# Optimization experiments

Hardware: AMD Instinct MI355X
Metric: run time of the kernel (lower is better)

The kernel has to match this reference:

```python
import jax, jax.numpy as jnp
import numpy as np

H, N, SEQ = 256, 64, 4096

def setup_inputs() -> dict:
    key = jax.random.key(0)
    kA, kB, kC, kdt = jax.random.split(key, 4)
    W = jax.random.normal(kA, (H, N, N), dtype=jnp.float32)
    # Hurwitz (stable) A: skew-symmetric part minus 0.5*I, like HiPPO-style stable transitions
    A = 0.5 * (W - jnp.swapaxes(W, -1, -2)) - 0.5 * jnp.eye(N, dtype=jnp.float32)
    B = jax.random.normal(kB, (H, N), dtype=jnp.float32)
    C = jax.random.normal(kC, (H, N), dtype=jnp.float32)
    # log_dt around log(0.01), matching typical S4 timescale init
    log_dt = jax.random.normal(kdt, (H,), dtype=jnp.float32) * 0.5 + jnp.log(0.01)
    return {"A": A, "B": B, "C": C, "log_dt": log_dt, "L": SEQ}

def _bilinear(dt, A, B):
    # dt: (H,), A: (H,N,N), B: (H,N)
    n = A.shape[-1]
    I = jnp.eye(n, dtype=A.dtype)
    A_back = I - (dt[:, None, None] / 2) * A   # (H,N,N)
    A_fwd = I + (dt[:, None, None] / 2) * A    # (H,N,N)
    dA = jnp.linalg.solve(A_back, A_fwd)                       # (H,N,N)
    dB = dt[:, None] * jnp.linalg.solve(A_back, B[..., None])[..., 0]  # (H,N)
    return dA, dB

def _krylov(L, dA, dB, C):
    # K[h, l] = C[h] @ dA[h]^l @ dB[h], computed by squaring/doubling
    x = dB[..., None]  # (H, N, 1)
    A_ = dA
    while x.shape[-1] < L:
        x2 = jnp.einsum('hmn,hnl->hml', A_, x)  # apply current power
        x = jnp.concatenate([x, x2], axis=-1)
        if x.shape[-1] < L:
            A_ = jnp.einsum('hmn,hnk->hmk', A_, A_)  # square the power
    x = x[..., :L]  # (H, N, L)
    return jnp.einsum('hn,hnl->hl', C, x)  # (H, L)

def reference(A, B, C, log_dt, L):
    dt = jnp.exp(log_dt)
    dA, dB = _bilinear(dt, A, B)
    return _krylov(L, dA, dB, C)
```

## Files before the change

### kernel.cpp

```cpp
#include <hip/hip_runtime.h>

constexpr int STRU = 68;

typedef short v8s __attribute__((ext_vector_type(8)));
typedef float v4f __attribute__((ext_vector_type(4)));

__device__ __forceinline__ unsigned packhl(float x) {
    unsigned xb = __builtin_bit_cast(unsigned, x);
    unsigned hb = xb & 0xffff0000u;
    float lof = x - __builtin_bit_cast(float, hb);
    unsigned lb = __builtin_bit_cast(unsigned, lof) + 0x8000u;
    return __builtin_amdgcn_perm(xb, lb, 0x07060302u);
}

__device__ __forceinline__ float unpackf(unsigned v) {
    float h = __builtin_bit_cast(float, v & 0xffff0000u);
    float l = __builtin_bit_cast(float, v << 16);
    return h + l;
}

__device__ __forceinline__ void load_frag(const unsigned* p, v8s& hi, v8s& lo) {
    uint4 a = *(const uint4*)p;
    uint4 b = *(const uint4*)(p + 4);
    uint4 hw, lw;
    hw.x = __builtin_amdgcn_perm(a.y, a.x, 0x07060302u);
    hw.y = __builtin_amdgcn_perm(a.w, a.z, 0x07060302u);
    hw.z = __builtin_amdgcn_perm(b.y, b.x, 0x07060302u);
    hw.w = __builtin_amdgcn_perm(b.w, b.z, 0x07060302u);
    lw.x = __builtin_amdgcn_perm(a.y, a.x, 0x05040100u);
    lw.y = __builtin_amdgcn_perm(a.w, a.z, 0x05040100u);
    lw.z = __builtin_amdgcn_perm(b.y, b.x, 0x05040100u);
    lw.w = __builtin_amdgcn_perm(b.w, b.z, 0x05040100u);
    hi = __builtin_bit_cast(v8s, hw);
    lo = __builtin_bit_cast(v8s, lw);
}

#define MFMA __builtin_amdgcn_mfma_f32_16x16x32_bf16

template<int MODE>
__device__ __forceinline__ void mm64(const unsigned* __restrict__ P,
                                     const unsigned* __restrict__ Q,
                                     unsigned* D, unsigned* DT, float* G,
                                     const unsigned* R, float ca, float cb,
                                     int tid) {
    const int lane = tid & 63, w = tid >> 6;
    const int nh = lane & 15, qh = lane >> 4;
    const int tr = w >> 1, tc0 = (w & 1) << 1;
    v4f acc[2] = {v4f{0,0,0,0}, v4f{0,0,0,0}};
    #pragma unroll
    for (int kk = 0; kk < 2; ++kk) {
        const int kc = kk * 32 + qh * 8;
        v8s ph, pl, q0h, q0l, q1h, q1l;
        load_frag(P + (tr * 16 + nh) * STRU + kc, ph, pl);
        load_frag(Q + (tc0 * 16 + nh) * STRU + kc, q0h, q0l);
        load_frag(Q + ((tc0 + 1) * 16 + nh) * STRU + kc, q1h, q1l);
        acc[0] = MFMA(ph, q0h, acc[0], 0, 0, 0);
        acc[0] = MFMA(ph, q0l, acc[0], 0, 0, 0);
        acc[0] = MFMA(pl, q0h, acc[0], 0, 0, 0);
        acc[1] = MFMA(ph, q1h, acc[1], 0, 0, 0);
        acc[1] = MFMA(ph, q1l, acc[1], 0, 0, 0);
        acc[1] = MFMA(pl, q1h, acc[1], 0, 0, 0);
    }
    const int row0 = tr * 16 + qh * 4;
    #pragma unroll
    for (int c = 0; c < 2; ++c) {
        const int col = (tc0 + c) * 16 + nh;
        if constexpr (MODE == 2) {
            #pragma unroll
            for (int e = 0; e < 4; ++e) G[(row0 + e) * 64 + col] = acc[c][e];
        } else if constexpr (MODE == 0) {
            #pragma unroll
            for (int e = 0; e < 4; ++e)
                D[(row0 + e) * STRU + col] = packhl(acc[c][e]);
        } else if constexpr (MODE == 1) {
            #pragma unroll
            for (int e = 0; e < 4; ++e) {
                float v = acc[c][e] + ((row0 + e) == col ? 1.0f : 0.0f);
                D[(row0 + e) * STRU + col] = packhl(v);
            }
        } else if constexpr (MODE == 3) {
            uint4 tp;
            #pragma unroll
            for (int e = 0; e < 4; ++e) {
                unsigned pk = packhl(acc[c][e]);
                D[(row0 + e) * STRU + col] = pk;
                ((unsigned*)&tp)[e] = pk;
            }
            *(uint4*)&DT[col * STRU + row0] = tp;
        } else if constexpr (MODE == 4) {
            #pragma unroll
            for (int e = 0; e < 4; ++e) {
                float dv = ca * acc[c][e];
                float dg = ((row0 + e) == col) ? 1.0f : 0.0f;
                D[(row0 + e) * STRU + col]  = packhl(dv);
                DT[(row0 + e) * STRU + col] = packhl(dv + dg);
            }
        } else if constexpr (MODE == 5) {
            #pragma unroll
            for (int e = 0; e < 4; ++e) {
                float t  = unpackf(R[(row0 + e) * STRU + col]);
                float dg = ((row0 + e) == col) ? 1.0f : 0.0f;
                float base = ca * t - dg;
                float sv   = cb * acc[c][e];
                D[(row0 + e) * STRU + col]  = packhl(base + sv);
                DT[(row0 + e) * STRU + col] = packhl(base - sv);
            }
        }
    }
}

__device__ __forceinline__ void dbl64(unsigned* Xt, const unsigned* M, int k, int tid) {
    const int lane = tid & 63, w = tid >> 6;
    const int nh = lane & 15, qh = lane >> 4;
    const int nt = (k + 15) >> 4;
    if (w < 4 * nt) {
        const int t = w >> 2, cb = w & 3;
        v4f acc = {0, 0, 0, 0};
        #pragma unroll
        for (int kk = 0; kk < 2; ++kk) {
            const int kc = kk * 32 + qh * 8;
            v8s ph, pl, mh, ml;
            load_frag(Xt + (t * 16 + nh) * STRU + kc, ph, pl);
            load_frag(M + (cb * 16 + nh) * STRU + kc, mh, ml);
            acc = MFMA(ph, mh, acc, 0, 0, 0);
            acc = MFMA(ph, ml, acc, 0, 0, 0);
            acc = MFMA(pl, mh, acc, 0, 0, 0);
        }
        #pragma unroll
        for (int e = 0; e < 4; ++e) {
            const int j = t * 16 + qh * 4 + e;
            if (j < k) Xt[(k + j) * STRU + cb * 16 + nh] = packhl(acc[e]);
        }
    }
}

__launch_bounds__(512)
__global__ void krylov_kernel(const float* __restrict__ A,
                              const float* __restrict__ Bv,
                              const float* __restrict__ Cv,
                              const float* __restrict__ logdt,
                              float* __restrict__ out)
{
    const int h    = blockIdx.x;
    const int tid  = threadIdx.x;
    const int lane = tid & 63;
    const int w    = tid >> 6;

    __shared__ __align__(16) unsigned SM[6][64 * STRU];
    __shared__ float Bl[64];

    const float dt = expf(logdt[h]);
    const float c  = 0.5f * dt;
    const float al = 1.0f + 0.5f * c;
    const float sd = -(c * c) / (al * al);
    const float c1 = 2.0f / al;
    const float c2 = 2.0f * c / (al * al);

    const float* Ah = A + (size_t)h * 4096;

    for (int idx = tid; idx < 1024; idx += 512) {
        const int r = idx >> 4, c0 = (idx & 15) * 4;
        float4 v = *(const float4*)(Ah + idx * 4);
        if (r == c0 + 0) v.x += 0.5f;
        if (r == c0 + 1) v.y += 0.5f;
        if (r == c0 + 2) v.z += 0.5f;
        if (r == c0 + 3) v.w += 0.5f;
        uint4 pk = make_uint4(packhl(v.x), packhl(v.y), packhl(v.z), packhl(v.w));
        *(uint4*)&SM[0][r * STRU + c0] = pk;
    }
    if (tid < 64) Bl[tid] = Bv[h * 64 + tid];
    else if (tid < 128) SM[5][tid - 64] = packhl(Cv[h * 64 + (tid - 64)]);
    __syncthreads();

    mm64<4>(SM[0], SM[0], SM[1], SM[2], nullptr, nullptr, sd, 0.f, tid);
    __syncthreads();
    mm64<1>(SM[1], SM[2], SM[3], nullptr, nullptr, nullptr, 0.f, 0.f, tid);
    __syncthreads();
    mm64<1>(SM[1], SM[3], SM[2], nullptr, nullptr, nullptr, 0.f, 0.f, tid);
    __syncthreads();
    mm64<1>(SM[1], SM[2], SM[3], nullptr, nullptr, nullptr, 0.f, 0.f, tid);
    __syncthreads();
    mm64<5>(SM[0], SM[3], SM[2], SM[1], nullptr, SM[3], c1, c2, tid);
    __syncthreads();

    if (w == 0) {
        const unsigned* Xr = SM[2] + lane * STRU;
        float acc = 0.0f;
        #pragma unroll
        for (int m4 = 0; m4 < 16; ++m4) {
            uint4 xv = *(const uint4*)(Xr + 4 * m4);
            float4 b4 = *(const float4*)&Bl[4 * m4];
            acc += unpackf(xv.x) * b4.x + unpackf(xv.y) * b4.y
                 + unpackf(xv.z) * b4.z + unpackf(xv.w) * b4.w;
        }
        SM[4][lane] = packhl(c * (acc + Bl[lane]));
    }
    __syncthreads();

    unsigned *bX = SM[2], *bXT = SM[1], *bN = SM[0], *bNT = SM[3];
    #pragma unroll 1
    for (int s = 0; s < 6; ++s) {
        mm64<3>(bX, bXT, bN, bNT, nullptr, nullptr, 0.f, 0.f, tid);
        dbl64(SM[4], bX, 1 << s, tid);
        __syncthreads();
        unsigned* t0 = bX;  bX  = bN;  bN  = t0;
        t0 = bXT; bXT = bNT; bNT = t0;
    }

    #pragma unroll 1
    for (int s = 0; s < 6; ++s) {
        if (s < 5) mm64<3>(bX, bXT, bN, bNT, nullptr, nullptr, 0.f, 0.f, tid);
        dbl64(SM[5], bXT, 1 << s, tid);
        __syncthreads();
        if (s < 5) {
            unsigned* t0 = bX;  bX  = bN;  bN  = t0;
            t0 = bXT; bXT = bNT; bNT = t0;
        }
    }

    mm64<2>(SM[5], SM[4], nullptr, nullptr, out + (size_t)h * 4096, nullptr,
            0.f, 0.f, tid);
}

extern "C" void kernel_launch(void* const* d_in, const int* in_sizes, int n_in,
                              void* d_out, int out_size, void* d_ws, size_t ws_size,
                              hipStream_t stream) {
    const float* A  = (const float*)d_in[0];
    const float* B  = (const float*)d_in[1];
    const float* C  = (const float*)d_in[2];
    const float* ld = (const float*)d_in[3];
    float* out = (float*)d_out;
    const int H = in_sizes[3];
    krylov_kernel<<<H, 512, 0, stream>>>(A, B, C, ld, out);
}
```

Before: 79.63 us.

## Restructure Krylov kernel with 1024 threads, swizzled LDS, column-fragment loads and fewer buffers

Rewrites the per-head kernel to launch 1024 threads so each wave computes one 16x16 tile, and replaces the padded LDS layout with an XOR-swizzled one. Transposed copies of matrices are dropped in favour of column-strided fragment loads. The LDS footprint shrinks from six to four matrix buffers. The dB solve is restructured into two matrix-vector products, and the two doubling loops are merged into one 12-step loop. MFMA accumulation is split across two accumulators. The aim is to cut LDS bank conflicts, transpose writes and LDS usage, and to raise parallelism per block, at the cost of strided scalar LDS reads for the column fragments and more threads contending at each barrier.

```diff
diff --git a/kernel.cpp b/kernel.cpp
--- a/kernel.cpp
+++ b/kernel.cpp
@@ -4,6 +4,10 @@
 
 typedef short v8s __attribute__((ext_vector_type(8)));
 typedef float v4f __attribute__((ext_vector_type(4)));
+
+__device__ __forceinline__ int swz(int i, int j) {
+    return i * STRU + (j ^ ((i & 8) << 1));
+}
 
 __device__ __forceinline__ unsigned packhl(float x) {
     unsigned xb = __builtin_bit_cast(unsigned, x);
@@ -35,106 +39,47 @@
     lo = __builtin_bit_cast(v8s, lw);
 }
 
-#define MFMA __builtin_amdgcn_mfma_f32_16x16x32_bf16
-
-template<int MODE>
-__device__ __forceinline__ void mm64(const unsigned* __restrict__ P,
-                                     const unsigned* __restrict__ Q,
-                                     unsigned* D, unsigned* DT, float* G,
-                                     const unsigned* R, float ca, float cb,
-                                     int tid) {
-    const int lane = tid & 63, w = tid >> 6;
-    const int nh = lane & 15, qh = lane >> 4;
-    const int tr = w >> 1, tc0 = (w & 1) << 1;
-    v4f acc[2] = {v4f{0,0,0,0}, v4f{0,0,0,0}};
+__device__ __forceinline__ void load_col_frag(const unsigned* Q, int col, int kbase,
+                                              v8s& hi, v8s& lo) {
+    unsigned x[8];
+    #pragma unroll
+    for (int j = 0; j < 8; ++j) x[j] = Q[swz(kbase + j, col)];
+    uint4 hw, lw;
+    hw.x = __builtin_amdgcn_perm(x[1], x[0], 0x07060302u);
+    hw.y = __builtin_amdgcn_perm(x[3], x[2], 0x07060302u);
+    hw.z = __builtin_amdgcn_perm(x[5], x[4], 0x07060302u);
+    hw.w = __builtin_amdgcn_perm(x[7], x[6], 0x07060302u);
+    lw.x = __builtin_amdgcn_perm(x[1], x[0], 0x05040100u);
+    lw.y = __builtin_amdgcn_perm(x[3], x[2], 0x05040100u);
+    lw.z = __builtin_amdgcn_perm(x[5], x[4], 0x05040100u);
+    lw.w = __builtin_amdgcn_perm(x[7], x[6], 0x05040100u);
+    hi = __builtin_bit_cast(v8s, hw);
+    lo = __builtin_bit_cast(v8s, lw);
+}
+
+#define MFMA16 __builtin_amdgcn_mfma_f32_16x16x32_bf16
+
+template<bool BCOL>
+__device__ __forceinline__ v4f tile16(const unsigned* __restrict__ P,
+                                      const unsigned* __restrict__ Q,
+                                      int rb, int cb, int lane) {
+    const int nh = lane & 15, qd = lane >> 4;
+    v4f a0 = {0, 0, 0, 0}, a1 = {0, 0, 0, 0};
     #pragma unroll
     for (int kk = 0; kk < 2; ++kk) {
-        const int kc = kk * 32 + qh * 8;
-        v8s ph, pl, q0h, q0l, q1h, q1l;
-        load_frag(P + (tr * 16 + nh) * STRU + kc, ph, pl);
-        load_frag(Q + (tc0 * 16 + nh) * STRU + kc, q0h, q0l);
-        load_frag(Q + ((tc0 + 1) * 16 + nh) * STRU + kc, q1h, q1l);
-        acc[0] = MFMA(ph, q0h, acc[0], 0, 0, 0);
-        acc[0] = MFMA(ph, q0l, acc[0], 0, 0, 0);
-        acc[0] = MFMA(pl, q0h, acc[0], 0, 0, 0);
-        acc[1] = MFMA(ph, q1h, acc[1], 0, 0, 0);
-        acc[1] = MFMA(ph, q1l, acc[1], 0, 0, 0);
-        acc[1] = MFMA(pl, q1h, acc[1], 0, 0, 0);
-    }
-    const int row0 = tr * 16 + qh * 4;
-    #pragma unroll
-    for (int c = 0; c < 2; ++c) {
-        const int col = (tc0 + c) * 16 + nh;
-        if constexpr (MODE == 2) {
-            #pragma unroll
-            for (int e = 0; e < 4; ++e) G[(row0 + e) * 64 + col] = acc[c][e];
-        } else if constexpr (MODE == 0) {
-            #pragma unroll
-            for (int e = 0; e < 4; ++e)
-                D[(row0 + e) * STRU + col] = packhl(acc[c][e]);
-        } else if constexpr (MODE == 1) {
-            #pragma unroll
-            for (int e = 0; e < 4; ++e) {
-                float v = acc[c][e] + ((row0 + e) == col ? 1.0f : 0.0f);
-                D[(row0 + e) * STRU + col] = packhl(v);
-            }
-        } else if constexpr (MODE == 3) {
-            uint4 tp;
-            #pragma unroll
-            for (int e = 0; e < 4; ++e) {
-                unsigned pk = packhl(acc[c][e]);
-                D[(row0 + e) * STRU + col] = pk;
-                ((unsigned*)&tp)[e] = pk;
-            }
-            *(uint4*)&DT[col * STRU + row0] = tp;
-        } else if constexpr (MODE == 4) {
-            #pragma unroll
-            for (int e = 0; e < 4; ++e) {
-                float dv = ca * acc[c][e];
-                float dg = ((row0 + e) == col) ? 1.0f : 0.0f;
-                D[(row0 + e) * STRU + col]  = packhl(dv);
-                DT[(row0 + e) * STRU + col] = packhl(dv + dg);
-            }
-        } else if constexpr (MODE == 5) {
-            #pragma unroll
-            for (int e = 0; e < 4; ++e) {
-                float t  = unpackf(R[(row0 + e) * STRU + col]);
-                float dg = ((row0 + e) == col) ? 1.0f : 0.0f;
-                float base = ca * t - dg;
-                float sv   = cb * acc[c][e];
-                D[(row0 + e) * STRU + col]  = packhl(base + sv);
-                DT[(row0 + e) * STRU + col] = packhl(base - sv);
-            }
-        }
-    }
-}
-
-__device__ __forceinline__ void dbl64(unsigned* Xt, const unsigned* M, int k, int tid) {
-    const int lane = tid & 63, w = tid >> 6;
-    const int nh = lane & 15, qh = lane >> 4;
-    const int nt = (k + 15) >> 4;
-    if (w < 4 * nt) {
-        const int t = w >> 2, cb = w & 3;
-        v4f acc = {0, 0, 0, 0};
-        #pragma unroll
-        for (int kk = 0; kk < 2; ++kk) {
-            const int kc = kk * 32 + qh * 8;
-            v8s ph, pl, mh, ml;
-            load_frag(Xt + (t * 16 + nh) * STRU + kc, ph, pl);
-            load_frag(M + (cb * 16 + nh) * STRU + kc, mh, ml);
-            acc = MFMA(ph, mh, acc, 0, 0, 0);
-            acc = MFMA(ph, ml, acc, 0, 0, 0);
-            acc = MFMA(pl, mh, acc, 0, 0, 0);
-        }
-        #pragma unroll
-        for (int e = 0; e < 4; ++e) {
-            const int j = t * 16 + qh * 4 + e;
-            if (j < k) Xt[(k + j) * STRU + cb * 16 + nh] = packhl(acc[e]);
-        }
-    }
-}
-
-__launch_bounds__(512)
+        const int kc = kk * 32 + qd * 8;
+        v8s ph, pl, qh, ql;
+        load_frag(P + swz(rb + nh, kc), ph, pl);
+        if constexpr (BCOL) load_col_frag(Q, cb + nh, kc, qh, ql);
+        else                load_frag(Q + swz(cb + nh, kc), qh, ql);
+        a0 = MFMA16(ph, qh, a0, 0, 0, 0);
+        a1 = MFMA16(ph, ql, a1, 0, 0, 0);
+        a1 = MFMA16(pl, qh, a1, 0, 0, 0);
+    }
+    return a0 + a1;
+}
+
+__launch_bounds__(1024)
 __global__ void krylov_kernel(const float* __restrict__ A,
                               const float* __restrict__ Bv,
                               const float* __restrict__ Cv,
@@ -145,81 +90,145 @@
     const int tid  = threadIdx.x;
     const int lane = tid & 63;
     const int w    = tid >> 6;
-
-    __shared__ __align__(16) unsigned SM[6][64 * STRU];
-    __shared__ float Bl[64];
-
-    const float dt = expf(logdt[h]);
-    const float c  = 0.5f * dt;
-    const float al = 1.0f + 0.5f * c;
-    const float sd = -(c * c) / (al * al);
-    const float c1 = 2.0f / al;
-    const float c2 = 2.0f * c / (al * al);
+    const int nh   = lane & 15, qd = lane >> 4;
+    const int rb   = (w >> 2) * 16, cb = (w & 3) * 16;
+
+    __shared__ __align__(16) unsigned W0[64 * STRU], W1[64 * STRU],
+                                      W2[64 * STRU], W3[64 * STRU];
+    __shared__ float Bl[64], Cl[64], tmv[64];
+
+    const float dt  = expf(logdt[h]);
+    const float c   = 0.5f * dt;
+    const float al  = 1.0f + 0.5f * c;
+    const float sd2 = (c * c) / (al * al);
+    const float c1  = 2.0f / al;
+    const float c2  = 2.0f * c / (al * al);
+    const float k1  = dt / al;
+    const float k2  = dt * c / (al * al);
 
     const float* Ah = A + (size_t)h * 4096;
 
-    for (int idx = tid; idx < 1024; idx += 512) {
-        const int r = idx >> 4, c0 = (idx & 15) * 4;
-        float4 v = *(const float4*)(Ah + idx * 4);
-        if (r == c0 + 0) v.x += 0.5f;
-        if (r == c0 + 1) v.y += 0.5f;
-        if (r == c0 + 2) v.z += 0.5f;
-        if (r == c0 + 3) v.w += 0.5f;
+    {
+        const int rr = tid >> 4, c0 = (tid & 15) * 4;
+        float4 v = *(const float4*)(Ah + rr * 64 + c0);
+        if (rr == c0 + 0) v.x += 0.5f;
+        if (rr == c0 + 1) v.y += 0.5f;
+        if (rr == c0 + 2) v.z += 0.5f;
+        if (rr == c0 + 3) v.w += 0.5f;
         uint4 pk = make_uint4(packhl(v.x), packhl(v.y), packhl(v.z), packhl(v.w));
-        *(uint4*)&SM[0][r * STRU + c0] = pk;
-    }
-    if (tid < 64) Bl[tid] = Bv[h * 64 + tid];
-    else if (tid < 128) SM[5][tid - 64] = packhl(Cv[h * 64 + (tid - 64)]);
-    __syncthreads();
-
-    mm64<4>(SM[0], SM[0], SM[1], SM[2], nullptr, nullptr, sd, 0.f, tid);
-    __syncthreads();
-    mm64<1>(SM[1], SM[2], SM[3], nullptr, nullptr, nullptr, 0.f, 0.f, tid);
-    __syncthreads();
-    mm64<1>(SM[1], SM[3], SM[2], nullptr, nullptr, nullptr, 0.f, 0.f, tid);
-    __syncthreads();
-    mm64<1>(SM[1], SM[2], SM[3], nullptr, nullptr, nullptr, 0.f, 0.f, tid);
-    __syncthreads();
-    mm64<5>(SM[0], SM[3], SM[2], SM[1], nullptr, SM[3], c1, c2, tid);
-    __syncthreads();
-
-    if (w == 0) {
-        const unsigned* Xr = SM[2] + lane * STRU;
-        float acc = 0.0f;
-        #pragma unroll
-        for (int m4 = 0; m4 < 16; ++m4) {
-            uint4 xv = *(const uint4*)(Xr + 4 * m4);
-            float4 b4 = *(const float4*)&Bl[4 * m4];
-            acc += unpackf(xv.x) * b4.x + unpackf(xv.y) * b4.y
-                 + unpackf(xv.z) * b4.z + unpackf(xv.w) * b4.w;
-        }
-        SM[4][lane] = packhl(c * (acc + Bl[lane]));
-    }
-    __syncthreads();
-
-    unsigned *bX = SM[2], *bXT = SM[1], *bN = SM[0], *bNT = SM[3];
+        *(uint4*)&W0[swz(rr, c0)] = pk;
+        if (tid < 64) Bl[tid] = Bv[h * 64 + tid];
+        else if (tid < 128) Cl[tid - 64] = Cv[h * 64 + (tid - 64)];
+    }
+    __syncthreads();
+
+    {
+        v4f a = tile16<true>(W0, W0, rb, cb, lane);
+        #pragma unroll
+        for (int e = 0; e < 4; ++e) {
+            const int row = rb + qd * 4 + e, col = cb + nh;
+            float dv = sd2 * a[e];
+            W1[swz(row, col)] = packhl(dv);
+            W2[swz(row, col)] = packhl(dv + (row == col ? 1.0f : 0.0f));
+        }
+    }
+    __syncthreads();
+    {
+        v4f a = tile16<true>(W1, W2, rb, cb, lane);
+        #pragma unroll
+        for (int e = 0; e < 4; ++e) {
+            const int row = rb + qd * 4 + e, col = cb + nh;
+            W3[swz(row, col)] = packhl(a[e] + (row == col ? 1.0f : 0.0f));
+        }
+    }
+    __syncthreads();
+    {
+        v4f a = tile16<true>(W1, W3, rb, cb, lane);
+        #pragma unroll
+        for (int e = 0; e < 4; ++e) {
+            const int row = rb + qd * 4 + e, col = cb + nh;
+            W2[swz(row, col)] = packhl(a[e] + (row == col ? 1.0f : 0.0f));
+        }
+    }
+    __syncthreads();
+    {
+        v4f a = tile16<true>(W1, W2, rb, cb, lane);
+        #pragma unroll
+        for (int e = 0; e < 4; ++e) {
+            const int row = rb + qd * 4 + e, col = cb + nh;
+            W3[swz(row, col)] = packhl(a[e] + (row == col ? 1.0f : 0.0f));
+        }
+    }
+    __syncthreads();
+    {
+        v4f a = tile16<true>(W0, W3, rb, cb, lane);
+        #pragma unroll
+        for (int e = 0; e < 4; ++e) {
+            const int row = rb + qd * 4 + e, col = cb + nh;
+            float t = unpackf(W3[swz(row, col)]);
+            W1[swz(row, col)] = packhl(c1 * t - (row == col ? 1.0f : 0.0f)
+                                       + c2 * a[e]);
+        }
+        if (w == 0) {
+            float acc1 = 0.0f;
+            #pragma unroll
+            for (int m4 = 0; m4 < 16; ++m4) {
+                uint4 tv = *(const uint4*)&W3[swz(lane, 4 * m4)];
+                float4 b4 = *(const float4*)&Bl[4 * m4];
+                acc1 += unpackf(tv.x) * b4.x + unpackf(tv.y) * b4.y
+                      + unpackf(tv.z) * b4.z + unpackf(tv.w) * b4.w;
+            }
+            tmv[lane] = acc1;
+            __threadfence_block();
+            float acc2 = 0.0f;
+            #pragma unroll
+            for (int m4 = 0; m4 < 16; ++m4) {
+                uint4 sv = *(const uint4*)&W0[swz(lane, 4 * m4)];
+                float4 t4 = *(const float4*)&tmv[4 * m4];
+                acc2 += unpackf(sv.x) * t4.x + unpackf(sv.y) * t4.y
+                      + unpackf(sv.z) * t4.z + unpackf(sv.w) * t4.w;
+            }
+            W2[swz(0, lane)] = packhl(k1 * acc1 + k2 * acc2);
+        }
+    }
+    __syncthreads();
+
+    unsigned* cur = W1;
+    unsigned* nxt = W0;
     #pragma unroll 1
-    for (int s = 0; s < 6; ++s) {
-        mm64<3>(bX, bXT, bN, bNT, nullptr, nullptr, 0.f, 0.f, tid);
-        dbl64(SM[4], bX, 1 << s, tid);
+    for (int s = 0; s < 12; ++s) {
+        if (s < 11) {
+            v4f a = tile16<true>(cur, cur, rb, cb, lane);
+            #pragma unroll
+            for (int e = 0; e < 4; ++e)
+                nxt[swz(rb + qd * 4 + e, cb + nh)] = packhl(a[e]);
+        }
+        const int p2 = (s < 6) ? s : s - 6;
+        const int k  = 1 << p2;
+        const int ndb = (k > 16) ? 8 : 4;
+        if (w < ndb) {
+            const int rt = (w >> 2) * 16, tc = (w & 3) * 16;
+            unsigned* Xt = (s < 6) ? W2 : W3;
+            v4f a = (s < 6) ? tile16<false>(Xt, cur, rt, tc, lane)
+                            : tile16<true >(Xt, cur, rt, tc, lane);
+            #pragma unroll
+            for (int e = 0; e < 4; ++e) {
+                const int j = rt + qd * 4 + e;
+                if (j < k) Xt[swz(k + j, tc + nh)] = packhl(a[e]);
+            }
+        }
+        if (s == 0 && w == 15) W3[swz(0, lane)] = packhl(Cl[lane]);
         __syncthreads();
-        unsigned* t0 = bX;  bX  = bN;  bN  = t0;
-        t0 = bXT; bXT = bNT; bNT = t0;
-    }
-
-    #pragma unroll 1
-    for (int s = 0; s < 6; ++s) {
-        if (s < 5) mm64<3>(bX, bXT, bN, bNT, nullptr, nullptr, 0.f, 0.f, tid);
-        dbl64(SM[5], bXT, 1 << s, tid);
-        __syncthreads();
-        if (s < 5) {
-            unsigned* t0 = bX;  bX  = bN;  bN  = t0;
-            t0 = bXT; bXT = bNT; bNT = t0;
-        }
-    }
-
-    mm64<2>(SM[5], SM[4], nullptr, nullptr, out + (size_t)h * 4096, nullptr,
-            0.f, 0.f, tid);
+        if (s < 11) { unsigned* t = cur; cur = nxt; nxt = t; }
+    }
+
+    {
+        v4f a = tile16<false>(W3, W2, rb, cb, lane);
+        float* oh = out + (size_t)h * 4096;
+        #pragma unroll
+        for (int e = 0; e < 4; ++e)
+            oh[(rb + qd * 4 + e) * 64 + cb + nh] = a[e];
+    }
 }
 
 extern "C" void kernel_launch(void* const* d_in, const int* in_sizes, int n_in,
@@ -231,5 +240,5 @@
     const float* ld = (const float*)d_in[3];
     float* out = (float*)d_out;
     const int H = in_sizes[3];
-    krylov_kernel<<<H, 512, 0, stream>>>(A, B, C, ld, out);
-}
+    krylov_kernel<<<H, 1024, 0, stream>>>(A, B, C, ld, out);
+}
```

Result: slower. 82.40 us (+3.5%).
